# Kernel tuning notes

Measured on AMD Instinct MI355X. Metric: run time of the kernel, lower is better.

The kernel has to match this reference:

```python
import jax, jax.numpy as jnp
import numpy as np

S_LEN, B, D = 1024, 32, 512
KD = VD = QD = HID = 512
KSZ = 3
EPS = 1e-12


def _l2norm(x):
    n = jnp.linalg.norm(x, axis=-1, keepdims=True)
    return x / jnp.maximum(n, EPS)


def _dwconv(x, w, b):
    # x: [B, C, S], w: [C, 1, K] (depthwise, groups=C), b: [C]
    pad = (KSZ - 1) // 2
    y = jax.lax.conv_general_dilated(
        x, w, window_strides=(1,), padding=[(pad, pad)],
        dimension_numbers=("NCH", "OIH", "NCH"), feature_group_count=x.shape[1])
    return y + b[None, :, None]


def _mem_mlp(x, W1, b1, W2, b2):
    h = jax.nn.silu(x @ W1.T + b1)
    return h @ W2.T + b2


def setup_inputs() -> dict:
    key = jax.random.key(0)
    ks = jax.random.split(key, 24)
    sc = 0.02
    inp = {"x": jax.random.normal(ks[0], (S_LEN, B, D), jnp.float32)}
    inp["Wk_w"] = jax.random.normal(ks[1], (KD, D)) * sc
    inp["Wk_b"] = jnp.zeros((KD,))
    inp["Wv_w"] = jax.random.normal(ks[2], (VD, D)) * sc
    inp["Wv_b"] = jnp.zeros((VD,))
    inp["Wq_w"] = jax.random.normal(ks[3], (QD, D)) * sc
    inp["Wq_b"] = jnp.zeros((QD,))
    inp["ck_w"] = jax.random.normal(ks[4], (KD, 1, KSZ)) * sc
    inp["ck_b"] = jnp.zeros((KD,))
    inp["cv_w"] = jax.random.normal(ks[5], (VD, 1, KSZ)) * sc
    inp["cv_b"] = jnp.zeros((VD,))
    inp["cq_w"] = jax.random.normal(ks[6], (QD, 1, KSZ)) * sc
    inp["cq_b"] = jnp.zeros((QD,))
    inp["M_W1"] = jax.random.normal(ks[7], (HID, KD)) * sc
    inp["M_b1"] = jnp.zeros((HID,))
    inp["M_W2"] = jax.random.normal(ks[8], (VD, HID)) * sc
    inp["M_b2"] = jnp.zeros((VD,))
    inp["a_w"] = jax.random.normal(ks[9], (1, D)) * sc
    inp["a_b"] = jnp.zeros((1,))
    inp["e_w"] = jax.random.normal(ks[10], (1, D)) * sc
    inp["e_b"] = jnp.zeros((1,))
    inp["t_w"] = jax.random.normal(ks[11], (1, D)) * sc
    inp["t_b"] = jnp.zeros((1,))
    return inp


def reference(x, Wk_w, Wk_b, Wv_w, Wv_b, Wq_w, Wq_b,
              ck_w, ck_b, cv_w, cv_b, cq_w, cq_b,
              M_W1, M_b1, M_W2, M_b2,
              a_w, a_b, e_w, e_b, t_w, t_b):
    # projections: x [S,B,D] -> [B,C,S] for depthwise conv, back to [S,B,C]
    def proj(W, bias, cw, cb):
        p = jnp.transpose(x @ W.T + bias, (1, 2, 0))  # [B,C,S]
        p = _dwconv(p, cw, cb)
        return jnp.transpose(p, (2, 0, 1))            # [S,B,C]

    keys = proj(Wk_w, Wk_b, ck_w, ck_b)
    values = proj(Wv_w, Wv_b, cv_w, cv_b)
    queries = proj(Wq_w, Wq_b, cq_w, cq_b)

    def inner_loss(params, kt, vt):
        W1, b1, W2, b2 = params
        pred = _mem_mlp(kt, W1, b1, W2, b2)
        return jnp.mean((pred - vt) ** 2)

    grad_loss = jax.grad(inner_loss)

    S0 = (jnp.zeros_like(M_W1), jnp.zeros_like(M_b1),
          jnp.zeros_like(M_W2), jnp.zeros_like(M_b2))

    def step(carry, inputs):
        M, S = carry
        xt, kt, vt, qt = inputs
        kt = _l2norm(kt)
        qt = _l2norm(qt)
        alpha = jnp.mean(jax.nn.sigmoid(xt @ a_w.T + a_b))
        eta = jnp.mean(jax.nn.sigmoid(xt @ e_w.T + e_b))
        theta = jnp.mean(jax.nn.softplus(xt @ t_w.T + t_b))
        # inner-loop 'surprise' gradient: detached from outer graph in torch
        g = grad_loss(jax.tree.map(jax.lax.stop_gradient, M),
                      jax.lax.stop_gradient(kt), jax.lax.stop_gradient(vt))
        g = jax.tree.map(jax.lax.stop_gradient, g)
        S_new = jax.tree.map(lambda s, gg: eta * s - theta * gg, S, g)
        M_new = jax.tree.map(lambda m, s: (1.0 - alpha) * m + s, M, S_new)
        retrieved = _mem_mlp(qt, *M_new)  # [B, VD]
        return (M_new, S_new), retrieved

    M0 = (M_W1, M_b1, M_W2, M_b2)
    (_, _), out = jax.lax.scan(step, (M0, S0), (x, keys, values, queries))
    return out  # [S, B, VD]
```

## Files before the change

### kernel.cpp

```cpp
#include <hip/hip_runtime.h>

#define NTHR 256
#define NBLK 256

#define GLOBAL_AS __attribute__((address_space(1)))
#define LDS_AS    __attribute__((address_space(3)))

#define VMCNT0()  asm volatile("s_waitcnt vmcnt(0)" ::: "memory")
#define VMCNT16() asm volatile("s_waitcnt vmcnt(16)" ::: "memory")

__device__ __forceinline__ float sigm_(float z) { return 1.f / (1.f + expf(-z)); }

__device__ __forceinline__ void coh_store(float* p, float v) {
    __hip_atomic_store(p, v, __ATOMIC_RELAXED, __HIP_MEMORY_SCOPE_AGENT);
}
__device__ __forceinline__ unsigned coh_loadu(const unsigned* p) {
    return __hip_atomic_load(p, __ATOMIC_RELAXED, __HIP_MEMORY_SCOPE_AGENT);
}

__device__ __forceinline__ void gbar(unsigned* arr, unsigned ep) {
    __syncthreads();
    if (threadIdx.x == 0) {
        asm volatile("s_waitcnt vmcnt(0)" ::: "memory");
        __hip_atomic_store(arr + blockIdx.x, ep, __ATOMIC_RELAXED, __HIP_MEMORY_SCOPE_AGENT);
    }
    if (blockIdx.x == 0) {
        if (threadIdx.x < 64) {
            const unsigned* a4 = arr + threadIdx.x * 4;
            for (;;) {
                unsigned m0 = coh_loadu(a4 + 0);
                unsigned m1 = coh_loadu(a4 + 1);
                unsigned m2 = coh_loadu(a4 + 2);
                unsigned m3 = coh_loadu(a4 + 3);
                bool ok = (m0 >= ep) & (m1 >= ep) & (m2 >= ep) & (m3 >= ep);
                if (__all(ok)) break;
                __builtin_amdgcn_s_sleep(1);
            }
            if (threadIdx.x == 0)
                __hip_atomic_store(arr + 320, ep, __ATOMIC_RELAXED, __HIP_MEMORY_SCOPE_AGENT);
        }
    } else if (threadIdx.x == 0) {
        while (coh_loadu(arr + 320) < ep) __builtin_amdgcn_s_sleep(1);
    }
    __syncthreads();
}

template <int AUX>
__device__ __forceinline__ void stage_dma(const float* __restrict__ src, float (*hb)[516], int tid) {
    const int lane = tid & 63;
    const int wbase = tid - lane;
#pragma unroll
    for (int l = 0; l < 16; ++l) {
        const int e0 = wbase + l * 256;
        const float* g = src + (size_t)(e0 + lane) * 4;
        float* d = &hb[e0 >> 7][(e0 & 127) << 2];
        __builtin_amdgcn_global_load_lds((const GLOBAL_AS unsigned int*)g,
                                         (LDS_AS unsigned int*)d, 16, 0, AUX);
    }
}

__global__ void proj_gemm(const float* __restrict__ A, const float* __restrict__ W,
                          const float* __restrict__ bias, float* __restrict__ C) {
    __shared__ float As[64][33];
    __shared__ float Ws[64][33];
    const int bn = blockIdx.x * 64, bc = blockIdx.y * 64;
    const int tx = threadIdx.x & 15, ty = threadIdx.x >> 4;
    float acc[4][4] = {};
    for (int k0 = 0; k0 < 512; k0 += 32) {
#pragma unroll
        for (int l = 0; l < 2; ++l) {
            int f4 = threadIdx.x + l * 256;
            int row = f4 >> 3;
            int kk = (f4 & 7) << 2;
            float4 av = *(const float4*)&A[(size_t)(bn + row) * 512 + k0 + kk];
            float4 wv = *(const float4*)&W[(size_t)(bc + row) * 512 + k0 + kk];
            As[row][kk] = av.x; As[row][kk + 1] = av.y; As[row][kk + 2] = av.z; As[row][kk + 3] = av.w;
            Ws[row][kk] = wv.x; Ws[row][kk + 1] = wv.y; Ws[row][kk + 2] = wv.z; Ws[row][kk + 3] = wv.w;
        }
        __syncthreads();
#pragma unroll
        for (int kk = 0; kk < 32; ++kk) {
            float a0 = As[ty * 4 + 0][kk], a1 = As[ty * 4 + 1][kk], a2 = As[ty * 4 + 2][kk], a3 = As[ty * 4 + 3][kk];
            float w0 = Ws[tx * 4 + 0][kk], w1 = Ws[tx * 4 + 1][kk], w2 = Ws[tx * 4 + 2][kk], w3 = Ws[tx * 4 + 3][kk];
            acc[0][0] += a0 * w0; acc[0][1] += a0 * w1; acc[0][2] += a0 * w2; acc[0][3] += a0 * w3;
            acc[1][0] += a1 * w0; acc[1][1] += a1 * w1; acc[1][2] += a1 * w2; acc[1][3] += a1 * w3;
            acc[2][0] += a2 * w0; acc[2][1] += a2 * w1; acc[2][2] += a2 * w2; acc[2][3] += a2 * w3;
            acc[3][0] += a3 * w0; acc[3][1] += a3 * w1; acc[3][2] += a3 * w2; acc[3][3] += a3 * w3;
        }
        __syncthreads();
    }
    float4 bvv = *(const float4*)&bias[bc + tx * 4];
#pragma unroll
    for (int i = 0; i < 4; ++i) {
        float4 o = make_float4(acc[i][0] + bvv.x, acc[i][1] + bvv.y, acc[i][2] + bvv.z, acc[i][3] + bvv.w);
        *(float4*)&C[(size_t)(bn + ty * 4 + i) * 512 + bc + tx * 4] = o;
    }
}

__global__ void conv_kernel(const float* __restrict__ P, const float* __restrict__ cw,
                            const float* __restrict__ cb, float* __restrict__ O) {
    int idx = blockIdx.x * 256 + threadIdx.x;
    if (idx >= 1024 * 32 * 128) return;
    int c4 = (idx & 127) << 2;
    int sb = idx >> 7;
    int s = sb >> 5, b = sb & 31;
    float acc0 = cb[c4 + 0], acc1 = cb[c4 + 1], acc2 = cb[c4 + 2], acc3 = cb[c4 + 3];
#pragma unroll
    for (int d = 0; d < 3; ++d) {
        int s2 = s + d - 1;
        if (s2 < 0 || s2 >= 1024) continue;
        float4 pv = *(const float4*)&P[((size_t)s2 * 32 + b) * 512 + c4];
        acc0 += pv.x * cw[(c4 + 0) * 3 + d];
        acc1 += pv.y * cw[(c4 + 1) * 3 + d];
        acc2 += pv.z * cw[(c4 + 2) * 3 + d];
        acc3 += pv.w * cw[(c4 + 3) * 3 + d];
    }
    *(float4*)&O[(size_t)sb * 512 + c4] = make_float4(acc0, acc1, acc2, acc3);
}

__global__ void scalars_kernel(const float* __restrict__ x,
                               const float* __restrict__ aw, const float* __restrict__ ab,
                               const float* __restrict__ ew, const float* __restrict__ eb,
                               const float* __restrict__ tw, const float* __restrict__ tb,
                               float* __restrict__ scal) {
    const int t = blockIdx.x, tid = threadIdx.x;
    const int b = tid >> 3, part = tid & 7;
    const float* xp = x + ((size_t)t * 32 + b) * 512 + part * 64;
    float sa = 0.f, se = 0.f, st = 0.f;
    for (int i = 0; i < 64; i += 4) {
        float4 xv = *(const float4*)&xp[i];
        float4 av = *(const float4*)&aw[part * 64 + i];
        float4 ev = *(const float4*)&ew[part * 64 + i];
        float4 tv = *(const float4*)&tw[part * 64 + i];
        sa += xv.x * av.x + xv.y * av.y + xv.z * av.z + xv.w * av.w;
        se += xv.x * ev.x + xv.y * ev.y + xv.z * ev.z + xv.w * ev.w;
        st += xv.x * tv.x + xv.y * tv.y + xv.z * tv.z + xv.w * tv.w;
    }
#pragma unroll
    for (int m = 1; m < 8; m <<= 1) {
        sa += __shfl_xor(sa, m);
        se += __shfl_xor(se, m);
        st += __shfl_xor(st, m);
    }
    __shared__ float ra[32], re[32], rt[32];
    if (part == 0) {
        ra[b] = sigm_(sa + ab[0]);
        re[b] = sigm_(se + eb[0]);
        float z = st + tb[0];
        rt[b] = fmaxf(z, 0.f) + log1pf(expf(-fabsf(z)));
    }
    __syncthreads();
    if (tid == 0) { float s = 0.f; for (int i = 0; i < 32; ++i) s += ra[i]; scal[t] = s / 32.f; }
    if (tid == 1) { float s = 0.f; for (int i = 0; i < 32; ++i) s += re[i]; scal[1024 + t] = s / 32.f; }
    if (tid == 2) { float s = 0.f; for (int i = 0; i < 32; ++i) s += rt[i]; scal[2048 + t] = s / 32.f; }
}

__global__ void l2norm_kernel(float* __restrict__ Kb, float* __restrict__ Qb) {
    int w = (blockIdx.x * 256 + threadIdx.x) >> 6;
    int lane = threadIdx.x & 63;
    if (w >= 2 * 32768) return;
    float* row = (w < 32768) ? (Kb + (size_t)w * 512) : (Qb + (size_t)(w - 32768) * 512);
    float4 v0 = *(float4*)&row[lane * 8];
    float4 v1 = *(float4*)&row[lane * 8 + 4];
    float ss = v0.x * v0.x + v0.y * v0.y + v0.z * v0.z + v0.w * v0.w
             + v1.x * v1.x + v1.y * v1.y + v1.z * v1.z + v1.w * v1.w;
#pragma unroll
    for (int m = 1; m < 64; m <<= 1) ss += __shfl_xor(ss, m);
    float inv = 1.f / fmaxf(sqrtf(ss), 1e-12f);
    v0.x *= inv; v0.y *= inv; v0.z *= inv; v0.w *= inv;
    v1.x *= inv; v1.y *= inv; v1.z *= inv; v1.w *= inv;
    *(float4*)&row[lane * 8] = v0;
    *(float4*)&row[lane * 8 + 4] = v1;
}

__global__ void __launch_bounds__(NTHR, 1) scan_kernel(
    const float* __restrict__ Kn, const float* __restrict__ Vv, const float* __restrict__ Qn,
    const float* __restrict__ scal,
    const float* __restrict__ MW1_0, const float* __restrict__ Mb1_0,
    const float* __restrict__ MW2_0, const float* __restrict__ Mb2_0,
    float* __restrict__ hG, float* __restrict__ dpG, float* __restrict__ h2G,
    float* __restrict__ outp, unsigned* __restrict__ bar) {
    const int g = blockIdx.x;
    const int tid = threadIdx.x;
    const int j0 = g * 2;
    unsigned ep = 0;

    __shared__ float W1[2][512], SW1[2][512];
    __shared__ float W2[2][512], SW2[2][512];
    __shared__ float W2T[2][512], SW2T[2][512];
    __shared__ float hbuf[32][516];
    __shared__ float buf2[32][516];
    __shared__ float red[4][32][2], red2[4][32][2];
    __shared__ float dpl[32][2], dzl[32][2], hj[32][2], hjp[32][2];
    __shared__ float bv1[2], Sb1[2], bv2[2], Sb2[2];

    for (int r = 0; r < 2; ++r) {
        for (int c = tid; c < 512; c += NTHR) {
            W1[r][c] = MW1_0[(size_t)(j0 + r) * 512 + c];
            W2[r][c] = MW2_0[(size_t)(j0 + r) * 512 + c];
            W2T[r][c] = MW2_0[(size_t)c * 512 + (j0 + r)];
            SW1[r][c] = 0.f; SW2[r][c] = 0.f; SW2T[r][c] = 0.f;
        }
    }
    if (tid < 2) { bv1[tid] = Mb1_0[j0 + tid]; Sb1[tid] = 0.f; bv2[tid] = Mb2_0[j0 + tid]; Sb2[tid] = 0.f; }
    __syncthreads();
    {
        const int b = tid & 31, r = (tid >> 5) & 1, q = tid >> 6;
        const float* kt = Kn + (size_t)b * 512;
        float p = 0.f;
        for (int i = q * 128; i < q * 128 + 128; i += 4) {
            float4 kv = *(const float4*)&kt[i];
            p += kv.x * W1[r][i] + kv.y * W1[r][i + 1] + kv.z * W1[r][i + 2] + kv.w * W1[r][i + 3];
        }
        red[q][b][r] = p;
    }
    __syncthreads();
    if (tid < 64) {
        const int b = tid & 31, r = tid >> 5;
        float z = red[0][b][r] + red[1][b][r] + red[2][b][r] + red[3][b][r] + bv1[r];
        hjp[b][r] = z;
        float hh = z * sigm_(z);
        hj[b][r] = hh;
        coh_store(&hG[b * 512 + j0 + r], hh);
    }
    gbar(bar, ++ep);

    for (int t = 0; t < 1024; ++t) {
        const float alpha = scal[t], eta = scal[1024 + t], theta = scal[2048 + t];
        float vpre = 0.f;
        if (tid < 64) vpre = Vv[((size_t)t * 32 + (tid & 31)) * 512 + j0 + (tid >> 5)];
        stage_dma<17>(hG, hbuf, tid);
        stage_dma<17>(h2G, buf2, tid);
        VMCNT0(); __syncthreads();
        {
            const int b = tid & 31, q = (tid >> 5) & 3, half = tid >> 7;
            float p0 = 0.f, p1 = 0.f;
            if (half == 0) {
                for (int j = q * 128; j < q * 128 + 128; j += 4) {
                    float4 hv = *(const float4*)&hbuf[b][j];
                    p0 += hv.x * W2[0][j] + hv.y * W2[0][j + 1] + hv.z * W2[0][j + 2] + hv.w * W2[0][j + 3];
                    p1 += hv.x * W2[1][j] + hv.y * W2[1][j + 1] + hv.z * W2[1][j + 2] + hv.w * W2[1][j + 3];
                }
                red[q][b][0] = p0; red[q][b][1] = p1;
            } else if (t > 0) {
                for (int j = q * 128; j < q * 128 + 128; j += 4) {
                    float4 hv = *(const float4*)&buf2[b][j];
                    p0 += hv.x * W2[0][j] + hv.y * W2[0][j + 1] + hv.z * W2[0][j + 2] + hv.w * W2[0][j + 3];
                    p1 += hv.x * W2[1][j] + hv.y * W2[1][j + 1] + hv.z * W2[1][j + 2] + hv.w * W2[1][j + 3];
                }
                red2[q][b][0] = p0; red2[q][b][1] = p1;
            }
        }
        __syncthreads();
        if (tid < 64) {
            const int b = tid & 31, o = tid >> 5;
            float pred = red[0][b][o] + red[1][b][o] + red[2][b][o] + red[3][b][o] + bv2[o];
            float dp = (pred - vpre) * (2.f / 16384.f);
            dpl[b][o] = dp;
            coh_store(&dpG[b * 512 + j0 + o], dp);
        } else if (tid < 128) {
            if (t > 0) {
                const int b = tid & 31, o = (tid >> 5) & 1;
                float ov = red2[0][b][o] + red2[1][b][o] + red2[2][b][o] + red2[3][b][o] + bv2[o];
                outp[((size_t)(t - 1) * 32 + b) * 512 + j0 + o] = ov;
            }
        }
        __syncthreads();
        if (tid < 2) {
            float db2 = 0.f;
            for (int b = 0; b < 32; ++b) db2 += dpl[b][tid];
            float s = eta * Sb2[tid] - theta * db2;
            Sb2[tid] = s;
            bv2[tid] = (1.f - alpha) * bv2[tid] + s;
        }
        {
            const int j = tid * 2;
            float d00 = 0.f, d01 = 0.f, d10 = 0.f, d11 = 0.f;
            for (int b = 0; b < 32; ++b) {
                float h0 = hbuf[b][j], h1 = hbuf[b][j + 1];
                float q0 = dpl[b][0], q1 = dpl[b][1];
                d00 += q0 * h0; d01 += q0 * h1; d10 += q1 * h0; d11 += q1 * h1;
            }
            float s;
            s = eta * SW2[0][j] - theta * d00;     SW2[0][j] = s;     W2[0][j]     = (1.f - alpha) * W2[0][j] + s;
            s = eta * SW2[0][j + 1] - theta * d01; SW2[0][j + 1] = s; W2[0][j + 1] = (1.f - alpha) * W2[0][j + 1] + s;
            s = eta * SW2[1][j] - theta * d10;     SW2[1][j] = s;     W2[1][j]     = (1.f - alpha) * W2[1][j] + s;
            s = eta * SW2[1][j + 1] - theta * d11; SW2[1][j + 1] = s; W2[1][j + 1] = (1.f - alpha) * W2[1][j + 1] + s;
        }
        gbar(bar, ++ep);

        stage_dma<17>(dpG, hbuf, tid);
        stage_dma<0>(Kn + (size_t)t * 16384, buf2, tid);
        VMCNT16(); __syncthreads();
        {
            const int b = tid & 31, r = (tid >> 5) & 1, q = tid >> 6;
            float p = 0.f;
            for (int o = q * 128; o < q * 128 + 128; o += 4) {
                float4 dv = *(const float4*)&hbuf[b][o];
                p += dv.x * W2T[r][o] + dv.y * W2T[r][o + 1] + dv.z * W2T[r][o + 2] + dv.w * W2T[r][o + 3];
            }
            red[q][b][r] = p;
        }
        __syncthreads();
        if (tid < 64) {
            const int b = tid & 31, r = tid >> 5;
            float dh = red[0][b][r] + red[1][b][r] + red[2][b][r] + red[3][b][r];
            float z = hjp[b][r];
            float sg = sigm_(z);
            dzl[b][r] = dh * (sg * (1.f + z * (1.f - sg)));
        }
        __syncthreads();
        if (tid < 2) {
            float db1 = 0.f;
            for (int b = 0; b < 32; ++b) db1 += dzl[b][tid];
            float s = eta * Sb1[tid] - theta * db1;
            Sb1[tid] = s;
            bv1[tid] = (1.f - alpha) * bv1[tid] + s;
        }
        {
            const int o = tid * 2;
            float d00 = 0.f, d01 = 0.f, d10 = 0.f, d11 = 0.f;
            for (int b = 0; b < 32; ++b) {
                float q0 = hbuf[b][o], q1 = hbuf[b][o + 1];
                float h0 = hj[b][0], h1 = hj[b][1];
                d00 += h0 * q0; d01 += h0 * q1; d10 += h1 * q0; d11 += h1 * q1;
            }
            float s;
            s = eta * SW2T[0][o] - theta * d00;     SW2T[0][o] = s;     W2T[0][o]     = (1.f - alpha) * W2T[0][o] + s;
            s = eta * SW2T[0][o + 1] - theta * d01; SW2T[0][o + 1] = s; W2T[0][o + 1] = (1.f - alpha) * W2T[0][o + 1] + s;
            s = eta * SW2T[1][o] - theta * d10;     SW2T[1][o] = s;     W2T[1][o]     = (1.f - alpha) * W2T[1][o] + s;
            s = eta * SW2T[1][o + 1] - theta * d11; SW2T[1][o + 1] = s; W2T[1][o + 1] = (1.f - alpha) * W2T[1][o + 1] + s;
        }
        __syncthreads();
        stage_dma<0>(Qn + (size_t)t * 16384, hbuf, tid);
        VMCNT16(); __syncthreads();
        {
            const int c = tid * 2;
            float d00 = 0.f, d01 = 0.f, d10 = 0.f, d11 = 0.f;
            for (int b = 0; b < 32; ++b) {
                float k0 = buf2[b][c], k1 = buf2[b][c + 1];
                float z0 = dzl[b][0], z1 = dzl[b][1];
                d00 += z0 * k0; d01 += z0 * k1; d10 += z1 * k0; d11 += z1 * k1;
            }
            float s;
            s = eta * SW1[0][c] - theta * d00;     SW1[0][c] = s;     W1[0][c]     = (1.f - alpha) * W1[0][c] + s;
            s = eta * SW1[0][c + 1] - theta * d01; SW1[0][c + 1] = s; W1[0][c + 1] = (1.f - alpha) * W1[0][c + 1] + s;
            s = eta * SW1[1][c] - theta * d10;     SW1[1][c] = s;     W1[1][c]     = (1.f - alpha) * W1[1][c] + s;
            s = eta * SW1[1][c + 1] - theta * d11; SW1[1][c + 1] = s; W1[1][c + 1] = (1.f - alpha) * W1[1][c + 1] + s;
        }
        __syncthreads();
        if (t < 1023) {
            stage_dma<0>(Kn + (size_t)(t + 1) * 16384, buf2, tid);
            VMCNT16();
        } else {
            VMCNT0();
        }
        __syncthreads();
        {
            const int b = tid & 31, r = (tid >> 5) & 1, q = tid >> 6;
            float p = 0.f;
            for (int i = q * 128; i < q * 128 + 128; i += 4) {
                float4 qv2 = *(const float4*)&hbuf[b][i];
                p += qv2.x * W1[r][i] + qv2.y * W1[r][i + 1] + qv2.z * W1[r][i + 2] + qv2.w * W1[r][i + 3];
            }
            red[q][b][r] = p;
        }
        __syncthreads();
        VMCNT0(); __syncthreads();
        if (t < 1023) {
            const int b = tid & 31, r = (tid >> 5) & 1, q = tid >> 6;
            float p = 0.f;
            for (int i = q * 128; i < q * 128 + 128; i += 4) {
                float4 kv2 = *(const float4*)&buf2[b][i];
                p += kv2.x * W1[r][i] + kv2.y * W1[r][i + 1] + kv2.z * W1[r][i + 2] + kv2.w * W1[r][i + 3];
            }
            red2[q][b][r] = p;
        }
        __syncthreads();
        if (tid < 64) {
            const int b = tid & 31, r = tid >> 5;
            float z2 = red[0][b][r] + red[1][b][r] + red[2][b][r] + red[3][b][r] + bv1[r];
            coh_store(&h2G[b * 512 + j0 + r], z2 * sigm_(z2));
            if (t < 1023) {
                float z = red2[0][b][r] + red2[1][b][r] + red2[2][b][r] + red2[3][b][r] + bv1[r];
                hjp[b][r] = z;
                float hh = z * sigm_(z);
                hj[b][r] = hh;
                coh_store(&hG[b * 512 + j0 + r], hh);
            }
        }
        gbar(bar, ++ep);
    }

    stage_dma<17>(h2G, hbuf, tid);
    VMCNT0(); __syncthreads();
    {
        const int b = tid & 31, q = (tid >> 5) & 3, half = tid >> 7;
        if (half == 0) {
            float p0 = 0.f, p1 = 0.f;
            for (int j = q * 128; j < q * 128 + 128; j += 4) {
                float4 hv = *(const float4*)&hbuf[b][j];
                p0 += hv.x * W2[0][j] + hv.y * W2[0][j + 1] + hv.z * W2[0][j + 2] + hv.w * W2[0][j + 3];
                p1 += hv.x * W2[1][j] + hv.y * W2[1][j + 1] + hv.z * W2[1][j + 2] + hv.w * W2[1][j + 3];
            }
            red[q][b][0] = p0; red[q][b][1] = p1;
        }
        __syncthreads();
        if (tid < 64) {
            const int b = tid & 31, o = tid >> 5;
            float ov = red[0][b][o] + red[1][b][o] + red[2][b][o] + red[3][b][o] + bv2[o];
            outp[((size_t)1023 * 32 + b) * 512 + j0 + o] = ov;
        }
    }
}

extern "C" void kernel_launch(void* const* d_in, const int* in_sizes, int n_in,
                              void* d_out, int out_size, void* d_ws, size_t ws_size,
                              hipStream_t stream) {
    (void)in_sizes; (void)n_in; (void)out_size; (void)ws_size;
    const float* x    = (const float*)d_in[0];
    const float* Wk_w = (const float*)d_in[1];
    const float* Wk_b = (const float*)d_in[2];
    const float* Wv_w = (const float*)d_in[3];
    const float* Wv_b = (const float*)d_in[4];
    const float* Wq_w = (const float*)d_in[5];
    const float* Wq_b = (const float*)d_in[6];
    const float* ck_w = (const float*)d_in[7];
    const float* ck_b = (const float*)d_in[8];
    const float* cv_w = (const float*)d_in[9];
    const float* cv_b = (const float*)d_in[10];
    const float* cq_w = (const float*)d_in[11];
    const float* cq_b = (const float*)d_in[12];
    const float* MW1  = (const float*)d_in[13];
    const float* Mb1  = (const float*)d_in[14];
    const float* MW2  = (const float*)d_in[15];
    const float* Mb2  = (const float*)d_in[16];
    const float* a_w  = (const float*)d_in[17];
    const float* a_b  = (const float*)d_in[18];
    const float* e_w  = (const float*)d_in[19];
    const float* e_b  = (const float*)d_in[20];
    const float* t_w  = (const float*)d_in[21];
    const float* t_b  = (const float*)d_in[22];

    float* out = (float*)d_out;
    float* ws = (float*)d_ws;
    float* Kb   = ws;
    float* Vb   = Kb + 16777216;
    float* Qb   = Vb + 16777216;
    float* scal = Qb + 16777216;
    float* hG   = scal + 3072;
    float* dpG  = hG + 16384;
    float* h2G  = dpG + 16384;
    unsigned* bar = (unsigned*)(h2G + 16384);
    float* tmp  = out;

    hipMemsetAsync(bar, 0, 8192, stream);
    scalars_kernel<<<1024, 256, 0, stream>>>(x, a_w, a_b, e_w, e_b, t_w, t_b, scal);
    proj_gemm<<<dim3(512, 8), 256, 0, stream>>>(x, Wk_w, Wk_b, tmp);
    conv_kernel<<<16384, 256, 0, stream>>>(tmp, ck_w, ck_b, Kb);
    proj_gemm<<<dim3(512, 8), 256, 0, stream>>>(x, Wv_w, Wv_b, tmp);
    conv_kernel<<<16384, 256, 0, stream>>>(tmp, cv_w, cv_b, Vb);
    proj_gemm<<<dim3(512, 8), 256, 0, stream>>>(x, Wq_w, Wq_b, tmp);
    conv_kernel<<<16384, 256, 0, stream>>>(tmp, cq_w, cq_b, Qb);
    l2norm_kernel<<<16384, 256, 0, stream>>>(Kb, Qb);

    const float *aKn = Kb, *aV = Vb, *aQn = Qb, *aSc = scal;
    const float *aW1 = MW1, *ab1 = Mb1, *aW2 = MW2, *ab2 = Mb2;
    float *ahG = hG, *adpG = dpG, *ah2G = h2G, *aout = out;
    unsigned* abar = bar;
    void* kargs[] = {(void*)&aKn, (void*)&aV, (void*)&aQn, (void*)&aSc,
                     (void*)&aW1, (void*)&ab1, (void*)&aW2, (void*)&ab2,
                     (void*)&ahG, (void*)&adpG, (void*)&ah2G, (void*)&aout, (void*)&abar};
    hipError_t ce = hipLaunchCooperativeKernel((void*)scan_kernel, dim3(NBLK), dim3(NTHR), kargs, 0, stream);
    if (ce != hipSuccess) {
        scan_kernel<<<dim3(NBLK), dim3(NTHR), 0, stream>>>(
            Kb, Vb, Qb, scal, MW1, Mb1, MW2, Mb2, hG, dpG, h2G, out, bar);
    }
}
```

Baseline: 15.83 ms.

## Double scan block threads and split grid barrier into arrive/wait phases

```diff
diff --git a/kernel.cpp b/kernel.cpp
--- a/kernel.cpp
+++ b/kernel.cpp
@@ -1,13 +1,13 @@
 #include <hip/hip_runtime.h>
 
-#define NTHR 256
+#define NTHR 512
 #define NBLK 256
 
 #define GLOBAL_AS __attribute__((address_space(1)))
 #define LDS_AS    __attribute__((address_space(3)))
 
-#define VMCNT0()  asm volatile("s_waitcnt vmcnt(0)" ::: "memory")
-#define VMCNT16() asm volatile("s_waitcnt vmcnt(16)" ::: "memory")
+#define VMCNT0() asm volatile("s_waitcnt vmcnt(0)" ::: "memory")
+#define VMCNT8() asm volatile("s_waitcnt vmcnt(8)" ::: "memory")
 
 __device__ __forceinline__ float sigm_(float z) { return 1.f / (1.f + expf(-z)); }
 
@@ -18,12 +18,13 @@
     return __hip_atomic_load(p, __ATOMIC_RELAXED, __HIP_MEMORY_SCOPE_AGENT);
 }
 
-__device__ __forceinline__ void gbar(unsigned* arr, unsigned ep) {
-    __syncthreads();
+__device__ __forceinline__ void gbar_arrive(unsigned* arr, unsigned ep) {
     if (threadIdx.x == 0) {
         asm volatile("s_waitcnt vmcnt(0)" ::: "memory");
         __hip_atomic_store(arr + blockIdx.x, ep, __ATOMIC_RELAXED, __HIP_MEMORY_SCOPE_AGENT);
     }
+}
+__device__ __forceinline__ void gbar_wait(unsigned* arr, unsigned ep) {
     if (blockIdx.x == 0) {
         if (threadIdx.x < 64) {
             const unsigned* a4 = arr + threadIdx.x * 4;
@@ -50,8 +51,8 @@
     const int lane = tid & 63;
     const int wbase = tid - lane;
 #pragma unroll
-    for (int l = 0; l < 16; ++l) {
-        const int e0 = wbase + l * 256;
+    for (int l = 0; l < 8; ++l) {
+        const int e0 = wbase + l * 512;
         const float* g = src + (size_t)(e0 + lane) * 4;
         float* d = &hb[e0 >> 7][(e0 & 127) << 2];
         __builtin_amdgcn_global_load_lds((const GLOBAL_AS unsigned int*)g,
@@ -190,12 +191,13 @@
     __shared__ float W2T[2][512], SW2T[2][512];
     __shared__ float hbuf[32][516];
     __shared__ float buf2[32][516];
-    __shared__ float red[4][32][2], red2[4][32][2];
+    __shared__ float red[8][32][2], red2[8][32][2];
     __shared__ float dpl[32][2], dzl[32][2], hj[32][2], hjp[32][2];
     __shared__ float bv1[2], Sb1[2], bv2[2], Sb2[2];
 
-    for (int r = 0; r < 2; ++r) {
-        for (int c = tid; c < 512; c += NTHR) {
+    for (int c = tid; c < 512; c += NTHR) {
+#pragma unroll
+        for (int r = 0; r < 2; ++r) {
             W1[r][c] = MW1_0[(size_t)(j0 + r) * 512 + c];
             W2[r][c] = MW2_0[(size_t)(j0 + r) * 512 + c];
             W2T[r][c] = MW2_0[(size_t)c * 512 + (j0 + r)];
@@ -208,7 +210,7 @@
         const int b = tid & 31, r = (tid >> 5) & 1, q = tid >> 6;
         const float* kt = Kn + (size_t)b * 512;
         float p = 0.f;
-        for (int i = q * 128; i < q * 128 + 128; i += 4) {
+        for (int i = q * 64; i < q * 64 + 64; i += 4) {
             float4 kv = *(const float4*)&kt[i];
             p += kv.x * W1[r][i] + kv.y * W1[r][i + 1] + kv.z * W1[r][i + 2] + kv.w * W1[r][i + 3];
         }
@@ -217,13 +219,16 @@
     __syncthreads();
     if (tid < 64) {
         const int b = tid & 31, r = tid >> 5;
-        float z = red[0][b][r] + red[1][b][r] + red[2][b][r] + red[3][b][r] + bv1[r];
+        float z = bv1[r];
+#pragma unroll
+        for (int q = 0; q < 8; ++q) z += red[q][b][r];
         hjp[b][r] = z;
         float hh = z * sigm_(z);
         hj[b][r] = hh;
         coh_store(&hG[b * 512 + j0 + r], hh);
     }
-    gbar(bar, ++ep);
+    __syncthreads();
+    ++ep; gbar_arrive(bar, ep); gbar_wait(bar, ep);
 
     for (int t = 0; t < 1024; ++t) {
         const float alpha = scal[t], eta = scal[1024 + t], theta = scal[2048 + t];
@@ -233,17 +238,17 @@
         stage_dma<17>(h2G, buf2, tid);
         VMCNT0(); __syncthreads();
         {
-            const int b = tid & 31, q = (tid >> 5) & 3, half = tid >> 7;
+            const int b = tid & 31, q = (tid >> 5) & 7;
             float p0 = 0.f, p1 = 0.f;
-            if (half == 0) {
-                for (int j = q * 128; j < q * 128 + 128; j += 4) {
+            if (tid < 256) {
+                for (int j = q * 64; j < q * 64 + 64; j += 4) {
                     float4 hv = *(const float4*)&hbuf[b][j];
                     p0 += hv.x * W2[0][j] + hv.y * W2[0][j + 1] + hv.z * W2[0][j + 2] + hv.w * W2[0][j + 3];
                     p1 += hv.x * W2[1][j] + hv.y * W2[1][j + 1] + hv.z * W2[1][j + 2] + hv.w * W2[1][j + 3];
                 }
                 red[q][b][0] = p0; red[q][b][1] = p1;
             } else if (t > 0) {
-                for (int j = q * 128; j < q * 128 + 128; j += 4) {
+                for (int j = q * 64; j < q * 64 + 64; j += 4) {
                     float4 hv = *(const float4*)&buf2[b][j];
                     p0 += hv.x * W2[0][j] + hv.y * W2[0][j + 1] + hv.z * W2[0][j + 2] + hv.w * W2[0][j + 3];
                     p1 += hv.x * W2[1][j] + hv.y * W2[1][j + 1] + hv.z * W2[1][j + 2] + hv.w * W2[1][j + 3];
@@ -254,18 +259,23 @@
         __syncthreads();
         if (tid < 64) {
             const int b = tid & 31, o = tid >> 5;
-            float pred = red[0][b][o] + red[1][b][o] + red[2][b][o] + red[3][b][o] + bv2[o];
+            float pred = bv2[o];
+#pragma unroll
+            for (int q = 0; q < 8; ++q) pred += red[q][b][o];
             float dp = (pred - vpre) * (2.f / 16384.f);
             dpl[b][o] = dp;
             coh_store(&dpG[b * 512 + j0 + o], dp);
         } else if (tid < 128) {
             if (t > 0) {
                 const int b = tid & 31, o = (tid >> 5) & 1;
-                float ov = red2[0][b][o] + red2[1][b][o] + red2[2][b][o] + red2[3][b][o] + bv2[o];
+                float ov = bv2[o];
+#pragma unroll
+                for (int q = 0; q < 8; ++q) ov += red2[q][b][o];
                 outp[((size_t)(t - 1) * 32 + b) * 512 + j0 + o] = ov;
             }
         }
         __syncthreads();
+        ++ep; gbar_arrive(bar, ep);
         if (tid < 2) {
             float db2 = 0.f;
             for (int b = 0; b < 32; ++b) db2 += dpl[b][tid];
@@ -274,28 +284,26 @@
             bv2[tid] = (1.f - alpha) * bv2[tid] + s;
         }
         {
-            const int j = tid * 2;
-            float d00 = 0.f, d01 = 0.f, d10 = 0.f, d11 = 0.f;
+            const int j = tid;
+            float d00 = 0.f, d10 = 0.f;
             for (int b = 0; b < 32; ++b) {
-                float h0 = hbuf[b][j], h1 = hbuf[b][j + 1];
-                float q0 = dpl[b][0], q1 = dpl[b][1];
-                d00 += q0 * h0; d01 += q0 * h1; d10 += q1 * h0; d11 += q1 * h1;
+                float h0 = hbuf[b][j];
+                d00 += dpl[b][0] * h0;
+                d10 += dpl[b][1] * h0;
             }
             float s;
-            s = eta * SW2[0][j] - theta * d00;     SW2[0][j] = s;     W2[0][j]     = (1.f - alpha) * W2[0][j] + s;
-            s = eta * SW2[0][j + 1] - theta * d01; SW2[0][j + 1] = s; W2[0][j + 1] = (1.f - alpha) * W2[0][j + 1] + s;
-            s = eta * SW2[1][j] - theta * d10;     SW2[1][j] = s;     W2[1][j]     = (1.f - alpha) * W2[1][j] + s;
-            s = eta * SW2[1][j + 1] - theta * d11; SW2[1][j + 1] = s; W2[1][j + 1] = (1.f - alpha) * W2[1][j + 1] + s;
-        }
-        gbar(bar, ++ep);
+            s = eta * SW2[0][j] - theta * d00; SW2[0][j] = s; W2[0][j] = (1.f - alpha) * W2[0][j] + s;
+            s = eta * SW2[1][j] - theta * d10; SW2[1][j] = s; W2[1][j] = (1.f - alpha) * W2[1][j] + s;
+        }
+        gbar_wait(bar, ep);
 
         stage_dma<17>(dpG, hbuf, tid);
         stage_dma<0>(Kn + (size_t)t * 16384, buf2, tid);
-        VMCNT16(); __syncthreads();
+        VMCNT8(); __syncthreads();
         {
             const int b = tid & 31, r = (tid >> 5) & 1, q = tid >> 6;
             float p = 0.f;
-            for (int o = q * 128; o < q * 128 + 128; o += 4) {
+            for (int o = q * 64; o < q * 64 + 64; o += 4) {
                 float4 dv = *(const float4*)&hbuf[b][o];
                 p += dv.x * W2T[r][o] + dv.y * W2T[r][o + 1] + dv.z * W2T[r][o + 2] + dv.w * W2T[r][o + 3];
             }
@@ -304,7 +312,9 @@
         __syncthreads();
         if (tid < 64) {
             const int b = tid & 31, r = tid >> 5;
-            float dh = red[0][b][r] + red[1][b][r] + red[2][b][r] + red[3][b][r];
+            float dh = 0.f;
+#pragma unroll
+            for (int q = 0; q < 8; ++q) dh += red[q][b][r];
             float z = hjp[b][r];
             float sg = sigm_(z);
             dzl[b][r] = dh * (sg * (1.f + z * (1.f - sg)));
@@ -318,40 +328,36 @@
             bv1[tid] = (1.f - alpha) * bv1[tid] + s;
         }
         {
-            const int o = tid * 2;
-            float d00 = 0.f, d01 = 0.f, d10 = 0.f, d11 = 0.f;
+            const int o = tid;
+            float d00 = 0.f, d10 = 0.f;
             for (int b = 0; b < 32; ++b) {
-                float q0 = hbuf[b][o], q1 = hbuf[b][o + 1];
-                float h0 = hj[b][0], h1 = hj[b][1];
-                d00 += h0 * q0; d01 += h0 * q1; d10 += h1 * q0; d11 += h1 * q1;
+                float q0 = hbuf[b][o];
+                d00 += hj[b][0] * q0;
+                d10 += hj[b][1] * q0;
             }
             float s;
-            s = eta * SW2T[0][o] - theta * d00;     SW2T[0][o] = s;     W2T[0][o]     = (1.f - alpha) * W2T[0][o] + s;
-            s = eta * SW2T[0][o + 1] - theta * d01; SW2T[0][o + 1] = s; W2T[0][o + 1] = (1.f - alpha) * W2T[0][o + 1] + s;
-            s = eta * SW2T[1][o] - theta * d10;     SW2T[1][o] = s;     W2T[1][o]     = (1.f - alpha) * W2T[1][o] + s;
-            s = eta * SW2T[1][o + 1] - theta * d11; SW2T[1][o + 1] = s; W2T[1][o + 1] = (1.f - alpha) * W2T[1][o + 1] + s;
+            s = eta * SW2T[0][o] - theta * d00; SW2T[0][o] = s; W2T[0][o] = (1.f - alpha) * W2T[0][o] + s;
+            s = eta * SW2T[1][o] - theta * d10; SW2T[1][o] = s; W2T[1][o] = (1.f - alpha) * W2T[1][o] + s;
         }
         __syncthreads();
         stage_dma<0>(Qn + (size_t)t * 16384, hbuf, tid);
-        VMCNT16(); __syncthreads();
-        {
-            const int c = tid * 2;
-            float d00 = 0.f, d01 = 0.f, d10 = 0.f, d11 = 0.f;
+        VMCNT8(); __syncthreads();
+        {
+            const int c = tid;
+            float d00 = 0.f, d10 = 0.f;
             for (int b = 0; b < 32; ++b) {
-                float k0 = buf2[b][c], k1 = buf2[b][c + 1];
-                float z0 = dzl[b][0], z1 = dzl[b][1];
-                d00 += z0 * k0; d01 += z0 * k1; d10 += z1 * k0; d11 += z1 * k1;
+                float k0 = buf2[b][c];
+                d00 += dzl[b][0] * k0;
+                d10 += dzl[b][1] * k0;
             }
             float s;
-            s = eta * SW1[0][c] - theta * d00;     SW1[0][c] = s;     W1[0][c]     = (1.f - alpha) * W1[0][c] + s;
-            s = eta * SW1[0][c + 1] - theta * d01; SW1[0][c + 1] = s; W1[0][c + 1] = (1.f - alpha) * W1[0][c + 1] + s;
-            s = eta * SW1[1][c] - theta * d10;     SW1[1][c] = s;     W1[1][c]     = (1.f - alpha) * W1[1][c] + s;
-            s = eta * SW1[1][c + 1] - theta * d11; SW1[1][c + 1] = s; W1[1][c + 1] = (1.f - alpha) * W1[1][c + 1] + s;
+            s = eta * SW1[0][c] - theta * d00; SW1[0][c] = s; W1[0][c] = (1.f - alpha) * W1[0][c] + s;
+            s = eta * SW1[1][c] - theta * d10; SW1[1][c] = s; W1[1][c] = (1.f - alpha) * W1[1][c] + s;
         }
         __syncthreads();
         if (t < 1023) {
             stage_dma<0>(Kn + (size_t)(t + 1) * 16384, buf2, tid);
-            VMCNT16();
+            VMCNT8();
         } else {
             VMCNT0();
         }
@@ -359,7 +365,7 @@
         {
             const int b = tid & 31, r = (tid >> 5) & 1, q = tid >> 6;
             float p = 0.f;
-            for (int i = q * 128; i < q * 128 + 128; i += 4) {
+            for (int i = q * 64; i < q * 64 + 64; i += 4) {
                 float4 qv2 = *(const float4*)&hbuf[b][i];
                 p += qv2.x * W1[r][i] + qv2.y * W1[r][i + 1] + qv2.z * W1[r][i + 2] + qv2.w * W1[r][i + 3];
             }
@@ -370,7 +376,7 @@
         if (t < 1023) {
             const int b = tid & 31, r = (tid >> 5) & 1, q = tid >> 6;
             float p = 0.f;
-            for (int i = q * 128; i < q * 128 + 128; i += 4) {
+            for (int i = q * 64; i < q * 64 + 64; i += 4) {
                 float4 kv2 = *(const float4*)&buf2[b][i];
                 p += kv2.x * W1[r][i] + kv2.y * W1[r][i + 1] + kv2.z * W1[r][i + 2] + kv2.w * W1[r][i + 3];
             }
@@ -379,38 +385,43 @@
         __syncthreads();
         if (tid < 64) {
             const int b = tid & 31, r = tid >> 5;
-            float z2 = red[0][b][r] + red[1][b][r] + red[2][b][r] + red[3][b][r] + bv1[r];
+            float z2 = bv1[r];
+#pragma unroll
+            for (int q = 0; q < 8; ++q) z2 += red[q][b][r];
             coh_store(&h2G[b * 512 + j0 + r], z2 * sigm_(z2));
             if (t < 1023) {
-                float z = red2[0][b][r] + red2[1][b][r] + red2[2][b][r] + red2[3][b][r] + bv1[r];
+                float z = bv1[r];
+#pragma unroll
+                for (int q = 0; q < 8; ++q) z += red2[q][b][r];
                 hjp[b][r] = z;
                 float hh = z * sigm_(z);
                 hj[b][r] = hh;
                 coh_store(&hG[b * 512 + j0 + r], hh);
             }
         }
-        gbar(bar, ++ep);
+        __syncthreads();
+        ++ep; gbar_arrive(bar, ep); gbar_wait(bar, ep);
     }
 
     stage_dma<17>(h2G, hbuf, tid);
     VMCNT0(); __syncthreads();
-    {
-        const int b = tid & 31, q = (tid >> 5) & 3, half = tid >> 7;
-        if (half == 0) {
-            float p0 = 0.f, p1 = 0.f;
-            for (int j = q * 128; j < q * 128 + 128; j += 4) {
-                float4 hv = *(const float4*)&hbuf[b][j];
-                p0 += hv.x * W2[0][j] + hv.y * W2[0][j + 1] + hv.z * W2[0][j + 2] + hv.w * W2[0][j + 3];
-                p1 += hv.x * W2[1][j] + hv.y * W2[1][j + 1] + hv.z * W2[1][j + 2] + hv.w * W2[1][j + 3];
-            }
-            red[q][b][0] = p0; red[q][b][1] = p1;
-        }
-        __syncthreads();
-        if (tid < 64) {
-            const int b = tid & 31, o = tid >> 5;
-            float ov = red[0][b][o] + red[1][b][o] + red[2][b][o] + red[3][b][o] + bv2[o];
-            outp[((size_t)1023 * 32 + b) * 512 + j0 + o] = ov;
-        }
+    if (tid < 256) {
+        const int b = tid & 31, q = (tid >> 5) & 7;
+        float p0 = 0.f, p1 = 0.f;
+        for (int j = q * 64; j < q * 64 + 64; j += 4) {
+            float4 hv = *(const float4*)&hbuf[b][j];
+            p0 += hv.x * W2[0][j] + hv.y * W2[0][j + 1] + hv.z * W2[0][j + 2] + hv.w * W2[0][j + 3];
+            p1 += hv.x * W2[1][j] + hv.y * W2[1][j + 1] + hv.z * W2[1][j + 2] + hv.w * W2[1][j + 3];
+        }
+        red[q][b][0] = p0; red[q][b][1] = p1;
+    }
+    __syncthreads();
+    if (tid < 64) {
+        const int b = tid & 31, o = tid >> 5;
+        float ov = bv2[o];
+#pragma unroll
+        for (int q = 0; q < 8; ++q) ov += red[q][b][o];
+        outp[((size_t)1023 * 32 + b) * 512 + j0 + o] = ov;
     }
 }
 
```

After: 14.84 ms. 1.07x faster.
